# Kernel optimization log

Hardware: AMD Instinct MI355X
Metric: run time of the kernel (lower is better)

## Reference

```python
import jax, jax.numpy as jnp
import numpy as np

NEG_INF = -1e30

def setup_inputs() -> dict:
    key = jax.random.key(0)
    ks = jax.random.split(key, 7)
    B, S, D = 2, 4096, 128
    scale = 1.0 / np.sqrt(D)
    return {
        "x": jax.random.normal(ks[0], (B, S, D), jnp.float32),
        "Wq": jax.random.normal(ks[1], (D, D), jnp.float32) * scale,
        "bq": jax.random.normal(ks[2], (D,), jnp.float32) * 0.01,
        "Wk": jax.random.normal(ks[3], (D, D), jnp.float32) * scale,
        "bk": jax.random.normal(ks[4], (D,), jnp.float32) * 0.01,
        "Wv": jax.random.normal(ks[5], (D, D), jnp.float32) * scale,
        "bv": jax.random.normal(ks[6], (D,), jnp.float32) * 0.01,
        "window_size": 128,
    }

def reference(x, Wq, bq, Wk, bk, Wv, bv, window_size):
    B, S, D = x.shape
    half = window_size // 2
    q = x @ Wq + bq
    k = x @ Wk + bk
    v = x @ Wv + bv
    # banded window indices: for query i, keys in [i-half, i+half]
    offs = jnp.arange(-half, half + 1)          # [W] with W = 2*half+1
    idx = jnp.arange(S)[:, None] + offs[None, :]  # [S, W]
    valid = (idx >= 0) & (idx < S)
    idxc = jnp.clip(idx, 0, S - 1)
    kw = k[:, idxc, :]  # [B, S, W, D]
    vw = v[:, idxc, :]  # [B, S, W, D]
    scores = jnp.einsum('bsd,bswd->bsw', q, kw) / jnp.sqrt(jnp.float32(D))
    scores = jnp.where(valid[None], scores, NEG_INF)
    attn = jax.nn.softmax(scores, axis=-1)
    out = jnp.einsum('bsw,bswd->bsd', attn, vw)
    return out
```

## Files before the change

kernel.cpp:

```cpp
#include <hip/hip_runtime.h>
#include <hip/hip_bf16.h>

typedef __attribute__((ext_vector_type(8))) short short8;
typedef __attribute__((ext_vector_type(4))) float f32x4;

union U16x8 { uint4 u; short8 s; unsigned short us[8]; };

#define S_LEN 4096
#define DH    128
#define TQ    16
#define VTS   168
#define PST   168
#define XSTR  136

__global__ __launch_bounds__(256) void qkv_kernel(
    const float* __restrict__ x,
    const float* __restrict__ Wq, const float* __restrict__ bq,
    const float* __restrict__ Wk, const float* __restrict__ bk,
    const float* __restrict__ Wv, const float* __restrict__ bv,
    __hip_bfloat16* __restrict__ q, __hip_bfloat16* __restrict__ k,
    __hip_bfloat16* __restrict__ v)
{
    __shared__ __align__(16) unsigned short XH[32 * XSTR];
    __shared__ __align__(16) unsigned short XL[32 * XSTR];

    const int t = threadIdx.x;
    const int row0 = blockIdx.x * 32;

    #pragma unroll
    for (int p = 0; p < 4; ++p) {
        int c = t + p * 256;
        int r = c >> 5, cg = c & 31;
        float4 xv = *(const float4*)(x + (size_t)(row0 + r) * DH + cg * 4);
        unsigned h[2], l[2];
        #pragma unroll
        for (int hw = 0; hw < 2; ++hw) {
            unsigned hh[2], ll[2];
            #pragma unroll
            for (int j = 0; j < 2; ++j) {
                float xs = (&xv.x)[hw * 2 + j];
                __hip_bfloat16 hb = __float2bfloat16(xs);
                float hf = __bfloat162float(hb);
                __hip_bfloat16 lb = __float2bfloat16(xs - hf);
                hh[j] = *(unsigned short*)&hb;
                ll[j] = *(unsigned short*)&lb;
            }
            h[hw] = hh[0] | (hh[1] << 16);
            l[hw] = ll[0] | (ll[1] << 16);
        }
        *(uint2*)&XH[r * XSTR + cg * 4] = make_uint2(h[0], h[1]);
        *(uint2*)&XL[r * XSTR + cg * 4] = make_uint2(l[0], l[1]);
    }
    __syncthreads();

    const int wave = t >> 6, lane = t & 63;
    const int i = lane & 15, g = lane >> 4;

    short8 ah[2][4], al[2][4];
    #pragma unroll
    for (int rt = 0; rt < 2; ++rt)
        #pragma unroll
        for (int kc = 0; kc < 4; ++kc) {
            ah[rt][kc] = *(const short8*)&XH[(rt*16 + i) * XSTR + kc*32 + g*8];
            al[rt][kc] = *(const short8*)&XL[(rt*16 + i) * XSTR + kc*32 + g*8];
        }

    const float* Ws[3] = {Wq, Wk, Wv};
    const float* Bs[3] = {bq, bk, bv};
    __hip_bfloat16* Os[3] = {q, k, v};

    #pragma unroll
    for (int mat = 0; mat < 3; ++mat) {
        #pragma unroll
        for (int ct = 0; ct < 2; ++ct) {
            const int col = wave*32 + ct*16 + i;
            const float bias = Bs[mat][col];

            short8 bf[4];
            #pragma unroll
            for (int kc = 0; kc < 4; ++kc) {
                const float* wp = Ws[mat] + (size_t)(kc*32 + g*8) * DH + col;
                U16x8 u;
                #pragma unroll
                for (int j = 0; j < 8; ++j) {
                    __hip_bfloat16 wb = __float2bfloat16(wp[(size_t)j * DH]);
                    u.us[j] = *(unsigned short*)&wb;
                }
                bf[kc] = u.s;
            }

            #pragma unroll
            for (int rt = 0; rt < 2; ++rt) {
                f32x4 acc; acc[0]=0.f; acc[1]=0.f; acc[2]=0.f; acc[3]=0.f;
                #pragma unroll
                for (int kc = 0; kc < 4; ++kc) {
                    acc = __builtin_amdgcn_mfma_f32_16x16x32_bf16(ah[rt][kc], bf[kc], acc, 0, 0, 0);
                    acc = __builtin_amdgcn_mfma_f32_16x16x32_bf16(al[rt][kc], bf[kc], acc, 0, 0, 0);
                }
                #pragma unroll
                for (int r = 0; r < 4; ++r) {
                    Os[mat][(size_t)(row0 + rt*16 + g*4 + r) * DH + col] =
                        __float2bfloat16(acc[r] + bias);
                }
            }
        }
    }
}

__device__ inline void vt_xpose_write(unsigned short* VT, const uint4* vr,
                                      int kgp, int dgp)
{
    unsigned w[8][4];
    #pragma unroll
    for (int p = 0; p < 4; ++p) {
        #pragma unroll
        for (int j = 0; j < 4; ++j) {
            unsigned xlo = ((const unsigned*)&vr[2*p])[j];
            unsigned ylo = ((const unsigned*)&vr[2*p+1])[j];
            w[2*j][p]   = __builtin_amdgcn_perm(ylo, xlo, 0x05040100u);
            w[2*j+1][p] = __builtin_amdgcn_perm(ylo, xlo, 0x07060302u);
        }
    }
    int sw = kgp + (dgp & 7); if (sw >= 21) sw -= 21;
    #pragma unroll
    for (int d = 0; d < 8; ++d) {
        int row = dgp*8 + d;
        *(uint4*)&VT[row*VTS + sw*8] =
            make_uint4(w[d][0], w[d][1], w[d][2], w[d][3]);
    }
}

__global__ __launch_bounds__(256) void attn_kernel(
    const __hip_bfloat16* __restrict__ qg,
    const __hip_bfloat16* __restrict__ kg,
    const __hip_bfloat16* __restrict__ vg,
    float* __restrict__ out, const int* __restrict__ wsz)
{
    __shared__ __align__(16) unsigned short VT[128 * VTS];
    __shared__ __align__(16) unsigned short Pm[TQ * PST];
    __shared__ float pmax[4][16];
    __shared__ float psum[4][16];

    const int t    = threadIdx.x;
    const int wave = t >> 6, lane = t & 63;
    const int i = lane & 15, g = lane >> 4;
    const int qblk = blockIdx.x;
    const int b    = qblk >> 8;
    const int s0   = (qblk & 255) * TQ;
    const int k0   = s0 - 64;
    const int half = wsz[0] >> 1;
    const float scale = 0.08838834764831845f;

    const __hip_bfloat16* kb = kg + (size_t)b * S_LEN * DH;
    const __hip_bfloat16* vb = vg + (size_t)b * S_LEN * DH;

    const int kgp0 = t >> 4, dgp0 = t & 15;
    const bool two = (t & 3) == 0;
    const int tau2 = 256 + (t >> 2);
    const int kgp1 = tau2 >> 4, dgp1 = tau2 & 15;
    uint4 vr0[8], vr1[8];
    #pragma unroll
    for (int r = 0; r < 8; ++r) {
        int key = k0 + kgp0*8 + r;
        uint4 val = make_uint4(0u,0u,0u,0u);
        if (key >= 0 && key < S_LEN)
            val = *(const uint4*)(vb + (size_t)key * DH + dgp0*8);
        vr0[r] = val;
    }
    #pragma unroll
    for (int r = 0; r < 8; ++r) {
        int key = k0 + kgp1*8 + r;
        uint4 val = make_uint4(0u,0u,0u,0u);
        if (two && key >= 0 && key < S_LEN)
            val = *(const uint4*)(vb + (size_t)key * DH + dgp1*8);
        vr1[r] = val;
    }

    short8 aq[4];
    {
        const __hip_bfloat16* qrow = qg + (size_t)(b * S_LEN + s0 + i) * DH;
        #pragma unroll
        for (int kc = 0; kc < 4; ++kc) {
            U16x8 u; u.u = *(const uint4*)(qrow + kc*32 + g*8);
            aq[kc] = u.s;
        }
    }

    const int nkt = (wave < 2) ? 3 : 2;
    f32x4 acc[3];
    #pragma unroll
    for (int u = 0; u < 3; ++u) { acc[u][0]=0.f; acc[u][1]=0.f; acc[u][2]=0.f; acc[u][3]=0.f; }
    #pragma unroll
    for (int u = 0; u < 3; ++u) {
        if (u < nkt) {
            int kt = wave + 4*u;
            int key = k0 + kt*16 + i;
            const __hip_bfloat16* krow = kb + (ptrdiff_t)key * DH;
            #pragma unroll
            for (int kc = 0; kc < 4; ++kc) {
                U16x8 u16v; u16v.u = *(const uint4*)(krow + kc*32 + g*8);
                acc[u] = __builtin_amdgcn_mfma_f32_16x16x32_bf16(aq[kc], u16v.s, acc[u], 0, 0, 0);
            }
        }
    }

    vt_xpose_write(VT, vr0, kgp0, dgp0);
    if (two) vt_xpose_write(VT, vr1, kgp1, dgp1);

    float sc[3][4], m4[4];
    #pragma unroll
    for (int r = 0; r < 4; ++r) m4[r] = -3e30f;
    #pragma unroll
    for (int u = 0; u < 3; ++u) {
        if (u < nkt) {
            int kt = wave + 4*u;
            int key = k0 + kt*16 + i;
            #pragma unroll
            for (int r = 0; r < 4; ++r) {
                int qrow = s0 + g*4 + r;
                bool valid = (key >= 0) && (key < S_LEN) &&
                             (key >= qrow - half) && (key <= qrow + half);
                float sv = valid ? acc[u][r] * scale : -1e30f;
                sc[u][r] = sv;
                m4[r] = fmaxf(m4[r], sv);
            }
        }
    }
    #pragma unroll
    for (int r = 0; r < 4; ++r) {
        #pragma unroll
        for (int m = 1; m < 16; m <<= 1)
            m4[r] = fmaxf(m4[r], __shfl_xor(m4[r], m, 64));
    }
    if (i == 0) {
        #pragma unroll
        for (int r = 0; r < 4; ++r) pmax[wave][g*4 + r] = m4[r];
    }
    __syncthreads();

    float M[4], l4[4];
    #pragma unroll
    for (int r = 0; r < 4; ++r) {
        int qr = g*4 + r;
        M[r] = fmaxf(fmaxf(pmax[0][qr], pmax[1][qr]), fmaxf(pmax[2][qr], pmax[3][qr]));
        l4[r] = 0.f;
    }
    #pragma unroll
    for (int u = 0; u < 3; ++u) {
        if (u < nkt) {
            int kt = wave + 4*u;
            #pragma unroll
            for (int r = 0; r < 4; ++r) {
                float p = __expf(sc[u][r] - M[r]);
                l4[r] += p;
                __hip_bfloat16 pb = __float2bfloat16(p);
                Pm[(g*4 + r) * PST + kt*16 + i] = *(unsigned short*)&pb;
            }
        }
    }
    #pragma unroll
    for (int r = 0; r < 4; ++r) {
        #pragma unroll
        for (int m = 1; m < 16; m <<= 1)
            l4[r] += __shfl_xor(l4[r], m, 64);
    }
    if (i == 0) {
        #pragma unroll
        for (int r = 0; r < 4; ++r) psum[wave][g*4 + r] = l4[r];
    }
    __syncthreads();

    float linv[4];
    #pragma unroll
    for (int r = 0; r < 4; ++r) {
        int qr = g*4 + r;
        linv[r] = 1.0f / (psum[0][qr] + psum[1][qr] + psum[2][qr] + psum[3][qr]);
    }

    short8 ap[5];
    #pragma unroll
    for (int kc = 0; kc < 5; ++kc)
        ap[kc] = *(const short8*)&Pm[i * PST + kc*32 + g*8];

    const int n0 = wave * 32;
    f32x4 oacc[2];
    #pragma unroll
    for (int nt = 0; nt < 2; ++nt) { oacc[nt][0]=0.f; oacc[nt][1]=0.f; oacc[nt][2]=0.f; oacc[nt][3]=0.f; }
    #pragma unroll
    for (int nt = 0; nt < 2; ++nt) {
        int row0 = n0 + nt*16 + i;
        int dgr = (row0 >> 3) & 7;
        #pragma unroll
        for (int kc = 0; kc < 5; ++kc) {
            int lg = 4*kc + g;
            int sw = lg + dgr; if (sw >= 21) sw -= 21;
            short8 bv = *(const short8*)&VT[row0 * VTS + sw*8];
            oacc[nt] = __builtin_amdgcn_mfma_f32_16x16x32_bf16(ap[kc], bv, oacc[nt], 0, 0, 0);
        }
    }

    #pragma unroll
    for (int nt = 0; nt < 2; ++nt) {
        #pragma unroll
        for (int r = 0; r < 4; ++r) {
            int qrow = s0 + g*4 + r;
            out[((size_t)(b * S_LEN) + qrow) * DH + n0 + nt*16 + i] = oacc[nt][r] * linv[r];
        }
    }
}

extern "C" void kernel_launch(void* const* d_in, const int* in_sizes, int n_in,
                              void* d_out, int out_size, void* d_ws, size_t ws_size,
                              hipStream_t stream) {
    const float* x  = (const float*)d_in[0];
    const float* Wq = (const float*)d_in[1];
    const float* bq = (const float*)d_in[2];
    const float* Wk = (const float*)d_in[3];
    const float* bk = (const float*)d_in[4];
    const float* Wv = (const float*)d_in[5];
    const float* bv = (const float*)d_in[6];
    const int* wsz  = (const int*)d_in[7];

    const int B = 2, S = 4096;
    const int N = B * S;

    __hip_bfloat16* q = (__hip_bfloat16*)d_ws;
    __hip_bfloat16* k = q + (size_t)N * DH;
    __hip_bfloat16* v = k + (size_t)N * DH;

    qkv_kernel<<<N / 32, 256, 0, stream>>>(x, Wq, bq, Wk, bk, Wv, bv, q, k, v);
    attn_kernel<<<N / TQ, 256, 0, stream>>>(q, k, v, (float*)d_out, wsz);
}
```

Measured before the change: 94.81 us.

## Split QKV projection into prep pass with transposed bf16 weights and remap attention blocks

A new prep kernel converts x to bf16 hi/lo split arrays in global memory and converts each weight matrix to bf16 in transposed layout through shared memory. The QKV kernel then uses a 2D grid with one projection matrix per blockIdx.y and loads contiguous short8 fragments, replacing strided scalar fp32 weight gathers and per-block conversion. The attention kernel's block index is permuted to interleave query blocks, which is meant to improve cache locality and scheduling. This adds an extra kernel launch and a global round trip for the hi/lo x arrays.

```diff
diff --git a/kernel.cpp b/kernel.cpp
--- a/kernel.cpp
+++ b/kernel.cpp
@@ -11,97 +11,115 @@
 #define TQ    16
 #define VTS   168
 #define PST   168
-#define XSTR  136
+
+__global__ __launch_bounds__(256) void prep_kernel(
+    const float* __restrict__ x,
+    const float* __restrict__ Wq, const float* __restrict__ Wk,
+    const float* __restrict__ Wv,
+    unsigned short* __restrict__ XH, unsigned short* __restrict__ XL,
+    unsigned short* __restrict__ WT)
+{
+    const int t = threadIdx.x;
+    const int bid = blockIdx.x;
+
+    __shared__ unsigned short T[128][136];
+
+    if (bid < 512) {
+        size_t off = ((size_t)bid * 256 + t) * 8;
+        float4 a = *(const float4*)(x + off);
+        float4 b = *(const float4*)(x + off + 4);
+        float xs[8] = {a.x, a.y, a.z, a.w, b.x, b.y, b.z, b.w};
+        U16x8 h, l;
+        #pragma unroll
+        for (int j = 0; j < 8; ++j) {
+            __hip_bfloat16 hb = __float2bfloat16(xs[j]);
+            float hf = __bfloat162float(hb);
+            __hip_bfloat16 lb = __float2bfloat16(xs[j] - hf);
+            h.us[j] = *(unsigned short*)&hb;
+            l.us[j] = *(unsigned short*)&lb;
+        }
+        *(uint4*)(XH + off) = h.u;
+        *(uint4*)(XL + off) = l.u;
+    } else {
+        const int mat = bid - 512;
+        const float* W = (mat == 0) ? Wq : (mat == 1) ? Wk : Wv;
+        unsigned short* WTm = WT + mat * (128 * 128);
+        #pragma unroll
+        for (int c = 0; c < 8; ++c) {
+            int linear = c * 2048 + t * 8;
+            int kk = linear >> 7, col = linear & 127;
+            float4 a = *(const float4*)(W + linear);
+            float4 b = *(const float4*)(W + linear + 4);
+            float ws[8] = {a.x, a.y, a.z, a.w, b.x, b.y, b.z, b.w};
+            #pragma unroll
+            for (int j = 0; j < 8; ++j) {
+                __hip_bfloat16 wb = __float2bfloat16(ws[j]);
+                T[kk][col + j] = *(unsigned short*)&wb;
+            }
+        }
+        __syncthreads();
+        #pragma unroll
+        for (int c = 0; c < 8; ++c) {
+            int linear = c * 2048 + t * 8;
+            int col = linear >> 7, k0 = linear & 127;
+            U16x8 u;
+            #pragma unroll
+            for (int j = 0; j < 8; ++j) u.us[j] = T[k0 + j][col];
+            *(uint4*)(WTm + linear) = u.u;
+        }
+    }
+}
 
 __global__ __launch_bounds__(256) void qkv_kernel(
-    const float* __restrict__ x,
-    const float* __restrict__ Wq, const float* __restrict__ bq,
-    const float* __restrict__ Wk, const float* __restrict__ bk,
-    const float* __restrict__ Wv, const float* __restrict__ bv,
+    const unsigned short* __restrict__ XH, const unsigned short* __restrict__ XL,
+    const unsigned short* __restrict__ WT,
+    const float* __restrict__ bq, const float* __restrict__ bk,
+    const float* __restrict__ bv,
     __hip_bfloat16* __restrict__ q, __hip_bfloat16* __restrict__ k,
     __hip_bfloat16* __restrict__ v)
 {
-    __shared__ __align__(16) unsigned short XH[32 * XSTR];
-    __shared__ __align__(16) unsigned short XL[32 * XSTR];
-
     const int t = threadIdx.x;
-    const int row0 = blockIdx.x * 32;
-
-    #pragma unroll
-    for (int p = 0; p < 4; ++p) {
-        int c = t + p * 256;
-        int r = c >> 5, cg = c & 31;
-        float4 xv = *(const float4*)(x + (size_t)(row0 + r) * DH + cg * 4);
-        unsigned h[2], l[2];
-        #pragma unroll
-        for (int hw = 0; hw < 2; ++hw) {
-            unsigned hh[2], ll[2];
-            #pragma unroll
-            for (int j = 0; j < 2; ++j) {
-                float xs = (&xv.x)[hw * 2 + j];
-                __hip_bfloat16 hb = __float2bfloat16(xs);
-                float hf = __bfloat162float(hb);
-                __hip_bfloat16 lb = __float2bfloat16(xs - hf);
-                hh[j] = *(unsigned short*)&hb;
-                ll[j] = *(unsigned short*)&lb;
-            }
-            h[hw] = hh[0] | (hh[1] << 16);
-            l[hw] = ll[0] | (ll[1] << 16);
-        }
-        *(uint2*)&XH[r * XSTR + cg * 4] = make_uint2(h[0], h[1]);
-        *(uint2*)&XL[r * XSTR + cg * 4] = make_uint2(l[0], l[1]);
-    }
-    __syncthreads();
-
     const int wave = t >> 6, lane = t & 63;
     const int i = lane & 15, g = lane >> 4;
+    const int row0 = blockIdx.x * 32;
+    const int mat = blockIdx.y;
+
+    const unsigned short* WTm = WT + mat * (128 * 128);
+    const float* bias_p = (mat == 0) ? bq : (mat == 1) ? bk : bv;
+    __hip_bfloat16* O = (mat == 0) ? q : (mat == 1) ? k : v;
 
     short8 ah[2][4], al[2][4];
     #pragma unroll
     for (int rt = 0; rt < 2; ++rt)
         #pragma unroll
         for (int kc = 0; kc < 4; ++kc) {
-            ah[rt][kc] = *(const short8*)&XH[(rt*16 + i) * XSTR + kc*32 + g*8];
-            al[rt][kc] = *(const short8*)&XL[(rt*16 + i) * XSTR + kc*32 + g*8];
-        }
-
-    const float* Ws[3] = {Wq, Wk, Wv};
-    const float* Bs[3] = {bq, bk, bv};
-    __hip_bfloat16* Os[3] = {q, k, v};
-
-    #pragma unroll
-    for (int mat = 0; mat < 3; ++mat) {
-        #pragma unroll
-        for (int ct = 0; ct < 2; ++ct) {
-            const int col = wave*32 + ct*16 + i;
-            const float bias = Bs[mat][col];
-
-            short8 bf[4];
+            size_t base = (size_t)(row0 + rt * 16 + i) * DH + kc * 32 + g * 8;
+            ah[rt][kc] = *(const short8*)(XH + base);
+            al[rt][kc] = *(const short8*)(XL + base);
+        }
+
+    #pragma unroll
+    for (int ct = 0; ct < 2; ++ct) {
+        const int col = wave * 32 + ct * 16 + i;
+        const float bias = bias_p[col];
+
+        short8 bf[4];
+        #pragma unroll
+        for (int kc = 0; kc < 4; ++kc)
+            bf[kc] = *(const short8*)(WTm + col * DH + kc * 32 + g * 8);
+
+        #pragma unroll
+        for (int rt = 0; rt < 2; ++rt) {
+            f32x4 acc; acc[0]=0.f; acc[1]=0.f; acc[2]=0.f; acc[3]=0.f;
             #pragma unroll
             for (int kc = 0; kc < 4; ++kc) {
-                const float* wp = Ws[mat] + (size_t)(kc*32 + g*8) * DH + col;
-                U16x8 u;
-                #pragma unroll
-                for (int j = 0; j < 8; ++j) {
-                    __hip_bfloat16 wb = __float2bfloat16(wp[(size_t)j * DH]);
-                    u.us[j] = *(unsigned short*)&wb;
-                }
-                bf[kc] = u.s;
-            }
-
-            #pragma unroll
-            for (int rt = 0; rt < 2; ++rt) {
-                f32x4 acc; acc[0]=0.f; acc[1]=0.f; acc[2]=0.f; acc[3]=0.f;
-                #pragma unroll
-                for (int kc = 0; kc < 4; ++kc) {
-                    acc = __builtin_amdgcn_mfma_f32_16x16x32_bf16(ah[rt][kc], bf[kc], acc, 0, 0, 0);
-                    acc = __builtin_amdgcn_mfma_f32_16x16x32_bf16(al[rt][kc], bf[kc], acc, 0, 0, 0);
-                }
-                #pragma unroll
-                for (int r = 0; r < 4; ++r) {
-                    Os[mat][(size_t)(row0 + rt*16 + g*4 + r) * DH + col] =
-                        __float2bfloat16(acc[r] + bias);
-                }
+                acc = __builtin_amdgcn_mfma_f32_16x16x32_bf16(ah[rt][kc], bf[kc], acc, 0, 0, 0);
+                acc = __builtin_amdgcn_mfma_f32_16x16x32_bf16(al[rt][kc], bf[kc], acc, 0, 0, 0);
+            }
+            #pragma unroll
+            for (int r = 0; r < 4; ++r) {
+                O[(size_t)(row0 + rt * 16 + g * 4 + r) * DH + col] =
+                    __float2bfloat16(acc[r] + bias);
             }
         }
     }
@@ -144,7 +162,8 @@
     const int t    = threadIdx.x;
     const int wave = t >> 6, lane = t & 63;
     const int i = lane & 15, g = lane >> 4;
-    const int qblk = blockIdx.x;
+    const int bid  = blockIdx.x;
+    const int qblk = (bid & 7) * 64 + (bid >> 3);
     const int b    = qblk >> 8;
     const int s0   = (qblk & 255) * TQ;
     const int k0   = s0 - 64;
@@ -327,7 +346,11 @@
     __hip_bfloat16* q = (__hip_bfloat16*)d_ws;
     __hip_bfloat16* k = q + (size_t)N * DH;
     __hip_bfloat16* v = k + (size_t)N * DH;
-
-    qkv_kernel<<<N / 32, 256, 0, stream>>>(x, Wq, bq, Wk, bk, Wv, bv, q, k, v);
+    unsigned short* XH = (unsigned short*)(v + (size_t)N * DH);
+    unsigned short* XL = XH + (size_t)N * DH;
+    unsigned short* WT = XL + (size_t)N * DH;
+
+    prep_kernel<<<515, 256, 0, stream>>>(x, Wq, Wk, Wv, XH, XL, WT);
+    qkv_kernel<<<dim3(256, 3), 256, 0, stream>>>(XH, XL, WT, bq, bk, bv, q, k, v);
     attn_kernel<<<N / TQ, 256, 0, stream>>>(q, k, v, (float*)d_out, wsz);
 }
```

New measurement: 96.82 us. 2.1% more time.
